# Kernel optimization log

Measured on AMD Instinct MI355X. Metric: run time of the kernel, lower is better.

Reference implementation:

```python
import jax, jax.numpy as jnp
import numpy as np

B, N, D, K = 16, 1024, 512, 32
EPS = 1e-12  # F.normalize default eps


def setup_inputs() -> dict:
    key = jax.random.key(0)
    k1, k2, k3 = jax.random.split(key, 3)
    x = jax.random.normal(k1, (B, N, D), dtype=jnp.float32)
    mask = (jax.random.uniform(k2, (B, N)) < 0.9).astype(jnp.float32)
    centroids = jax.random.uniform(k3, (D, K), dtype=jnp.float32)
    # _init_params: conv.weight = 2*alpha*centroids, conv.bias = -alpha*||centroids||_col
    W = 2.0 * centroids
    b = -jnp.linalg.norm(centroids, axis=0)
    return {"x": x, "mask": mask, "W": W, "b": b, "centroids": centroids}


def reference(x, mask, W, b, centroids):
    # descriptor-wise L2 normalization (normalize_input=True)
    xn = x / jnp.maximum(jnp.linalg.norm(x, axis=2, keepdims=True), EPS)
    # 1x1 conv (matmul) + bias, masked logits
    logits = (jnp.einsum('bnd,dk->bnk', xn, W) + b) * mask[:, :, None]
    soft_assign = jax.nn.softmax(logits, axis=2) * mask[:, :, None]  # (B,N,K)
    # entropy with -log2(0) -> 0 (matches log_p[isinf]=0 since sa*0 = 0 there)
    safe = jnp.where(soft_assign > 0, soft_assign, 1.0)
    assign_entropy = -(soft_assign * jnp.log2(safe)).sum() / mask.sum()
    # cluster-usage distribution
    assign_sum = soft_assign.sum(axis=1)  # (B,K)
    assign_dist = jax.nn.log_softmax(assign_sum, axis=1)
    # NetVLAD residual pooling, algebraically fused (avoids (B,N,D,K) tensor):
    # vlad[b,d,k] = sum_n xn*sa - centroids[d,k]*sum_n sa
    vlad = jnp.einsum('bnd,bnk->bdk', xn, soft_assign) - centroids[None] * assign_sum[:, None, :]
    vlad = vlad / jnp.maximum(jnp.linalg.norm(vlad, axis=1, keepdims=True), EPS)
    vlad = jnp.transpose(vlad, (0, 2, 1))  # (B,K,D)
    return (vlad, assign_dist, assign_entropy)
```

## Files before the change

kernel.cpp:

```cpp
#include <hip/hip_runtime.h>
#include <math.h>

#define B 16
#define N 1024
#define D 512
#define K 32
#define EPSF 1e-12f

#define WS_TT_F   0
#define WS_ASP_F  262144
#define WS_ENTP_F 294912
#define WS_MSKP_F 295936
#define WS_PART_F 296960

#define OFF_DIST 262144
#define OFF_ENT  262656

typedef __attribute__((ext_vector_type(8))) short s16x8;
typedef __attribute__((ext_vector_type(4))) short s16x4;
typedef __attribute__((ext_vector_type(4))) float f32x4;

__device__ __forceinline__ ushort f2b(float f) {
    unsigned u = __builtin_bit_cast(unsigned, f);
    u += 0x7fffu + ((u >> 16) & 1u);
    return (ushort)(u >> 16);
}

__global__ __launch_bounds__(256) void kA(const float* __restrict__ x,
    const float* __restrict__ mask, const float* __restrict__ Wf,
    const float* __restrict__ bias, float* __restrict__ ws)
{
    __shared__ ushort wtl[32 * 512];
    __shared__ ushort xs[4 * 16 * 128];
    __shared__ float4 accsh[2 * 128];
    __shared__ float ssqsh[2 * 16];
    __shared__ float invsh[2 * 16];
    const int bid = blockIdx.x;
    const int b = bid >> 5;
    const int s = bid & 31;
    const int tid = threadIdx.x;
    const int w = tid >> 6;
    const int rw = w & 1, dw = w >> 1;
    const int l = tid & 63;
    const int g = l >> 4, lo = l & 15;
    const int n0 = s * 32 + rw * 16;
    const int p = bid * 2 + rw;

    {
        const float4* Wg = (const float4*)Wf;
        #pragma unroll
        for (int i = 0; i < 16; ++i) {
            int f4 = tid + i * 256;
            float4 v = Wg[f4];
            int d = f4 >> 3, k4 = (f4 & 7) << 2;
            float vv[4] = {v.x, v.y, v.z, v.w};
            #pragma unroll
            for (int j = 0; j < 4; ++j) {
                int k = k4 + j;
                wtl[(k * 512 + d) ^ ((k & 7) << 3)] = f2b(vv[j]);
            }
        }
    }

    ushort* xw = xs + w * 2048;
    float ssq[8] = {0.f, 0.f, 0.f, 0.f, 0.f, 0.f, 0.f, 0.f};
    f32x4 acc[2] = {{0.f, 0.f, 0.f, 0.f}, {0.f, 0.f, 0.f, 0.f}};
    const float4* xg = (const float4*)(x + (size_t)(b * N + n0) * D);
    __syncthreads();

    #pragma unroll
    for (int cc = 0; cc < 2; ++cc) {
        const int c = dw * 2 + cc;
        float4 fv[8];
        #pragma unroll
        for (int j = 0; j < 8; ++j) {
            int idx = l + 64 * j;
            fv[j] = xg[(idx >> 5) * 128 + c * 32 + (idx & 31)];
        }
        #pragma unroll
        for (int j = 0; j < 8; ++j)
            ssq[j] += fv[j].x * fv[j].x + fv[j].y * fv[j].y
                    + fv[j].z * fv[j].z + fv[j].w * fv[j].w;
        #pragma unroll
        for (int j = 0; j < 8; ++j) {
            int idx = l + 64 * j;
            int r = idx >> 5, c4 = idx & 31;
            unsigned bo = (unsigned)(c4 * 8) ^ (unsigned)((r & 7) << 4);
            s16x4 sv = { (short)f2b(fv[j].x), (short)f2b(fv[j].y),
                         (short)f2b(fv[j].z), (short)f2b(fv[j].w) };
            *(s16x4*)&xw[r * 128 + (bo >> 1)] = sv;
        }
        __syncthreads();
        #pragma unroll
        for (int ks = 0; ks < 4; ++ks) {
            unsigned bo = (unsigned)(ks * 64 + g * 16) ^ (unsigned)((lo & 7) << 4);
            s16x8 bfrag = *(const s16x8*)&xw[lo * 128 + (bo >> 1)];
            int dglob = c * 128 + ks * 32 + g * 8;
            s16x8 a0 = *(const s16x8*)&wtl[(lo * 512 + dglob) ^ ((lo & 7) << 3)];
            s16x8 a1 = *(const s16x8*)&wtl[((16 + lo) * 512 + dglob) ^ ((lo & 7) << 3)];
            acc[0] = __builtin_amdgcn_mfma_f32_16x16x32_bf16(a0, bfrag, acc[0], 0, 0, 0);
            acc[1] = __builtin_amdgcn_mfma_f32_16x16x32_bf16(a1, bfrag, acc[1], 0, 0, 0);
        }
        __syncthreads();
    }

    #pragma unroll
    for (int j = 0; j < 8; ++j) {
        #pragma unroll
        for (int m = 16; m; m >>= 1) ssq[j] += __shfl_xor(ssq[j], m);
    }
    if (dw == 1) {
        if ((l & 31) == 0) {
            #pragma unroll
            for (int j = 0; j < 8; ++j)
                ssqsh[rw * 16 + (l >> 5) + 2 * j] = ssq[j];
        }
        accsh[rw * 128 + l * 2 + 0] = *(float4*)&acc[0];
        accsh[rw * 128 + l * 2 + 1] = *(float4*)&acc[1];
    }
    __syncthreads();
    if (dw == 0) {
        float4 o0 = accsh[rw * 128 + l * 2 + 0];
        float4 o1 = accsh[rw * 128 + l * 2 + 1];
        acc[0][0] += o0.x; acc[0][1] += o0.y; acc[0][2] += o0.z; acc[0][3] += o0.w;
        acc[1][0] += o1.x; acc[1][1] += o1.y; acc[1][2] += o1.z; acc[1][3] += o1.w;
        if ((l & 31) == 0) {
            #pragma unroll
            for (int j = 0; j < 8; ++j) {
                int r = (l >> 5) + 2 * j;
                invsh[rw * 16 + r] = 1.f / fmaxf(sqrtf(ssq[j] + ssqsh[rw * 16 + r]), EPSF);
            }
        }
    }
    __syncthreads();
    float sa[2][4];
    if (dw == 0) {
        const float inv = invsh[rw * 16 + lo];
        const float mv = mask[b * N + n0 + lo];
        float lg[2][4];
        #pragma unroll
        for (int kt = 0; kt < 2; ++kt)
            #pragma unroll
            for (int r = 0; r < 4; ++r)
                lg[kt][r] = (acc[kt][r] * inv + bias[kt * 16 + g * 4 + r]) * mv;
        float mx = lg[0][0];
        #pragma unroll
        for (int kt = 0; kt < 2; ++kt)
            #pragma unroll
            for (int r = 0; r < 4; ++r) mx = fmaxf(mx, lg[kt][r]);
        mx = fmaxf(mx, __shfl_xor(mx, 16));
        mx = fmaxf(mx, __shfl_xor(mx, 32));
        float e[2][4], sum = 0.f;
        #pragma unroll
        for (int kt = 0; kt < 2; ++kt)
            #pragma unroll
            for (int r = 0; r < 4; ++r) { e[kt][r] = __expf(lg[kt][r] - mx); sum += e[kt][r]; }
        sum += __shfl_xor(sum, 16);
        sum += __shfl_xor(sum, 32);
        const float rs = mv / sum;
        float ent = 0.f;
        #pragma unroll
        for (int kt = 0; kt < 2; ++kt)
            #pragma unroll
            for (int r = 0; r < 4; ++r) {
                sa[kt][r] = e[kt][r] * rs;
                ent += sa[kt][r] > 0.f ? -sa[kt][r] * __log2f(sa[kt][r]) : 0.f;
            }
        #pragma unroll
        for (int m = 32; m; m >>= 1) ent += __shfl_xor(ent, m);
        if (l == 0) ws[WS_ENTP_F + p] = ent;
        float mp = mv;
        #pragma unroll
        for (int m = 8; m; m >>= 1) mp += __shfl_xor(mp, m);
        if (l == 0) ws[WS_MSKP_F + p] = mp;
        #pragma unroll
        for (int kt = 0; kt < 2; ++kt)
            #pragma unroll
            for (int r = 0; r < 4; ++r) {
                float av = sa[kt][r];
                #pragma unroll
                for (int m = 8; m; m >>= 1) av += __shfl_xor(av, m);
                if (lo == 0) ws[WS_ASP_F + p * 32 + kt * 16 + g * 4 + r] = av;
            }
        #pragma unroll
        for (int kt = 0; kt < 2; ++kt)
            #pragma unroll
            for (int r = 0; r < 4; ++r)
                xw[(kt * 16 + g * 4 + r) * 16 + lo] = f2b(sa[kt][r] * inv);
    }
    __syncthreads();
    if (dw == 0) {
        ushort* tTg = (ushort*)ws;
        s16x8 tv = *(const s16x8*)&xw[l * 8];
        *(s16x8*)(tTg + (size_t)(b * 32 + (l >> 1)) * 1024 + n0 + (l & 1) * 8) = tv;
    }
}

__global__ __launch_bounds__(256) void kB(const float* __restrict__ x,
    const float* __restrict__ ws, float* __restrict__ parts)
{
    const int bid = blockIdx.x;
    const int b = bid >> 5;
    const int s = (bid >> 2) & 7;
    const int dh = bid & 3;
    const int w = threadIdx.x >> 6;
    const int l = threadIdx.x & 63;
    const int g = l >> 4, lo = l & 15;
    const int d0 = dh * 128 + w * 32;
    const ushort* tT = (const ushort*)ws;

    f32x4 acc[2][2] = {{{0.f,0.f,0.f,0.f},{0.f,0.f,0.f,0.f}},
                       {{0.f,0.f,0.f,0.f},{0.f,0.f,0.f,0.f}}};
    for (int ks = 0; ks < 4; ++ks) {
        int nb = s * 128 + ks * 32 + g * 8;
        s16x8 av[2];
        av[0] = *(const s16x8*)(tT + (size_t)(b * 32 + lo) * 1024 + nb);
        av[1] = *(const s16x8*)(tT + (size_t)(b * 32 + 16 + lo) * 1024 + nb);
        s16x8 bv[2];
        #pragma unroll
        for (int dt = 0; dt < 2; ++dt)
            #pragma unroll
            for (int j = 0; j < 8; ++j)
                bv[dt][j] = (short)f2b(x[(size_t)(b * N + nb + j) * 512 + d0 + dt * 16 + lo]);
        #pragma unroll
        for (int kt = 0; kt < 2; ++kt)
            #pragma unroll
            for (int dt = 0; dt < 2; ++dt)
                acc[kt][dt] = __builtin_amdgcn_mfma_f32_16x16x32_bf16(av[kt], bv[dt], acc[kt][dt], 0, 0, 0);
    }
    #pragma unroll
    for (int kt = 0; kt < 2; ++kt)
        #pragma unroll
        for (int dt = 0; dt < 2; ++dt)
            #pragma unroll
            for (int r = 0; r < 4; ++r) {
                int k = kt * 16 + g * 4 + r;
                int d = d0 + dt * 16 + lo;
                parts[((size_t)(s * 16 + b) * 32 + k) * 512 + d] = acc[kt][dt][r];
            }
}

__global__ __launch_bounds__(256) void kC(const float* __restrict__ cent,
    const float* __restrict__ ws, float* __restrict__ out)
{
    __shared__ float pm[256];
    __shared__ float asL[32];
    __shared__ float red[4];
    __shared__ float scs;
    const int bid = blockIdx.x;
    const int b = bid >> 5, k = bid & 31;
    const int t = threadIdx.x;
    {
        int kk = t & 31, i = t >> 5;
        float a = 0.f;
        #pragma unroll
        for (int ii = 0; ii < 8; ++ii)
            a += ws[WS_ASP_F + (size_t)(b * 64 + ii * 8 + i) * 32 + kk];
        pm[t] = a;
    }
    __syncthreads();
    if (t < 32) {
        float a = 0.f;
        #pragma unroll
        for (int i = 0; i < 8; ++i) a += pm[i * 32 + t];
        asL[t] = a;
    }
    __syncthreads();
    if (k == 0 && t < 32) {
        float a = asL[t];
        float mx = a;
        #pragma unroll
        for (int m = 16; m; m >>= 1) mx = fmaxf(mx, __shfl_xor(mx, m));
        float e = __expf(a - mx), ssum = e;
        #pragma unroll
        for (int m = 16; m; m >>= 1) ssum += __shfl_xor(ssum, m);
        out[OFF_DIST + b * 32 + t] = a - mx - logf(ssum);
    }
    if (bid == 0 && (t >> 6) == 1) {
        int l = t & 63;
        float es = 0.f, ms = 0.f;
        for (int i = l; i < 1024; i += 64) {
            es += ws[WS_ENTP_F + i];
            ms += ws[WS_MSKP_F + i];
        }
        #pragma unroll
        for (int m = 32; m; m >>= 1) { es += __shfl_xor(es, m); ms += __shfl_xor(ms, m); }
        if (l == 0) out[OFF_ENT] = es / ms;
    }
    const float as = asL[k];
    float v0 = 0.f, v1 = 0.f;
    #pragma unroll
    for (int s = 0; s < 8; ++s) {
        const float* pp = ws + WS_PART_F + ((size_t)(s * 16 + b) * 32 + k) * 512;
        v0 += pp[t];
        v1 += pp[t + 256];
    }
    v0 -= cent[t * 32 + k] * as;
    v1 -= cent[(t + 256) * 32 + k] * as;
    float ss = v0 * v0 + v1 * v1;
    #pragma unroll
    for (int m = 32; m; m >>= 1) ss += __shfl_xor(ss, m);
    if ((t & 63) == 0) red[t >> 6] = ss;
    __syncthreads();
    if (t == 0) scs = 1.f / fmaxf(sqrtf(red[0] + red[1] + red[2] + red[3]), EPSF);
    __syncthreads();
    out[(size_t)(b * 32 + k) * 512 + t] = v0 * scs;
    out[(size_t)(b * 32 + k) * 512 + t + 256] = v1 * scs;
}

extern "C" void kernel_launch(void* const* d_in, const int* in_sizes, int n_in,
                              void* d_out, int out_size, void* d_ws, size_t ws_size,
                              hipStream_t stream)
{
    const float* x    = (const float*)d_in[0];
    const float* mask = (const float*)d_in[1];
    const float* W    = (const float*)d_in[2];
    const float* bias = (const float*)d_in[3];
    const float* cent = (const float*)d_in[4];
    float* out = (float*)d_out;
    float* ws  = (float*)d_ws;

    kA<<<dim3(512), dim3(256), 0, stream>>>(x, mask, W, bias, ws);
    kB<<<dim3(512), dim3(256), 0, stream>>>(x, ws, ws + WS_PART_F);
    kC<<<dim3(512), dim3(256), 0, stream>>>(cent, ws, out);
}
```

Measured before the change: 33.99 us.

## Fuse VLAD aggregation into assignment kernel and precompute transposed weights

Moves the xn·soft_assign aggregation into the first kernel using a transposed bf16 copy of the x tile kept in LDS, eliminating the separate kernel that re-read x from global memory. A small prep kernel converts W to bf16 [K][D] and transposes centroids once, so kA no longer rebuilds the weight tile in LDS per block. Partials are now stored as bf16 with 32 splits and reduced in a narrower final kernel with vectorized loads. This trades higher LDS usage, more partial traffic and bf16 rounding of partial sums for removing a full pass over x.

```diff
diff --git a/kernel.cpp b/kernel.cpp
--- a/kernel.cpp
+++ b/kernel.cpp
@@ -7,11 +7,12 @@
 #define K 32
 #define EPSF 1e-12f
 
-#define WS_TT_F   0
-#define WS_ASP_F  262144
-#define WS_ENTP_F 294912
-#define WS_MSKP_F 295936
-#define WS_PART_F 296960
+#define WS_WT_F   0
+#define WS_CT_F   8192
+#define WS_ASP_F  24576
+#define WS_ENTP_F 57344
+#define WS_MSKP_F 58368
+#define WS_PART_F 59392
 
 #define OFF_DIST 262144
 #define OFF_ENT  262656
@@ -25,16 +26,49 @@
     u += 0x7fffu + ((u >> 16) & 1u);
     return (ushort)(u >> 16);
 }
-
-__global__ __launch_bounds__(256) void kA(const float* __restrict__ x,
-    const float* __restrict__ mask, const float* __restrict__ Wf,
-    const float* __restrict__ bias, float* __restrict__ ws)
+__device__ __forceinline__ float b2f(ushort u) {
+    return __builtin_bit_cast(float, (unsigned)u << 16);
+}
+
+__global__ __launch_bounds__(256) void k0_prep(const float* __restrict__ Wf,
+    const float* __restrict__ cent, float* __restrict__ ws)
 {
-    __shared__ ushort wtl[32 * 512];
-    __shared__ ushort xs[4 * 16 * 128];
+    const int t = threadIdx.x;
+    const int kk = t >> 3, dseg = (t & 7) * 64;
+    if (blockIdx.x == 0) {
+        ushort* wt = (ushort*)(ws + WS_WT_F);
+        #pragma unroll
+        for (int d8 = 0; d8 < 8; ++d8) {
+            s16x8 v;
+            #pragma unroll
+            for (int e = 0; e < 8; ++e)
+                v[e] = f2b(Wf[(dseg + d8 * 8 + e) * 32 + kk]);
+            *(s16x8*)(wt + kk * 512 + dseg + d8 * 8) = v;
+        }
+    } else {
+        float* ct = ws + WS_CT_F;
+        #pragma unroll
+        for (int d4 = 0; d4 < 16; ++d4) {
+            float4 v;
+            v.x = cent[(dseg + d4 * 4 + 0) * 32 + kk];
+            v.y = cent[(dseg + d4 * 4 + 1) * 32 + kk];
+            v.z = cent[(dseg + d4 * 4 + 2) * 32 + kk];
+            v.w = cent[(dseg + d4 * 4 + 3) * 32 + kk];
+            *(float4*)(ct + kk * 512 + dseg + d4 * 4) = v;
+        }
+    }
+}
+
+__global__ __launch_bounds__(256, 2) void kA(const float* __restrict__ x,
+    const float* __restrict__ mask, const float* __restrict__ bias,
+    float* __restrict__ ws, ushort* __restrict__ parts)
+{
+    __shared__ ushort xs[4 * 2048];
+    __shared__ ushort xsT[512 * 36];
+    __shared__ ushort tls[32 * 32];
     __shared__ float4 accsh[2 * 128];
-    __shared__ float ssqsh[2 * 16];
-    __shared__ float invsh[2 * 16];
+    __shared__ float ssqsh[32], invsh[32];
+
     const int bid = blockIdx.x;
     const int b = bid >> 5;
     const int s = bid & 31;
@@ -45,28 +79,12 @@
     const int g = l >> 4, lo = l & 15;
     const int n0 = s * 32 + rw * 16;
     const int p = bid * 2 + rw;
-
-    {
-        const float4* Wg = (const float4*)Wf;
-        #pragma unroll
-        for (int i = 0; i < 16; ++i) {
-            int f4 = tid + i * 256;
-            float4 v = Wg[f4];
-            int d = f4 >> 3, k4 = (f4 & 7) << 2;
-            float vv[4] = {v.x, v.y, v.z, v.w};
-            #pragma unroll
-            for (int j = 0; j < 4; ++j) {
-                int k = k4 + j;
-                wtl[(k * 512 + d) ^ ((k & 7) << 3)] = f2b(vv[j]);
-            }
-        }
-    }
+    const ushort* wt = (const ushort*)(ws + WS_WT_F);
 
     ushort* xw = xs + w * 2048;
     float ssq[8] = {0.f, 0.f, 0.f, 0.f, 0.f, 0.f, 0.f, 0.f};
     f32x4 acc[2] = {{0.f, 0.f, 0.f, 0.f}, {0.f, 0.f, 0.f, 0.f}};
     const float4* xg = (const float4*)(x + (size_t)(b * N + n0) * D);
-    __syncthreads();
 
     #pragma unroll
     for (int cc = 0; cc < 2; ++cc) {
@@ -89,19 +107,23 @@
             s16x4 sv = { (short)f2b(fv[j].x), (short)f2b(fv[j].y),
                          (short)f2b(fv[j].z), (short)f2b(fv[j].w) };
             *(s16x4*)&xw[r * 128 + (bo >> 1)] = sv;
-        }
-        __syncthreads();
+            int nn = rw * 16 + r;
+            int dbase = c * 128 + c4 * 4;
+            xsT[(dbase + 0) * 36 + nn] = (ushort)sv[0];
+            xsT[(dbase + 1) * 36 + nn] = (ushort)sv[1];
+            xsT[(dbase + 2) * 36 + nn] = (ushort)sv[2];
+            xsT[(dbase + 3) * 36 + nn] = (ushort)sv[3];
+        }
         #pragma unroll
         for (int ks = 0; ks < 4; ++ks) {
             unsigned bo = (unsigned)(ks * 64 + g * 16) ^ (unsigned)((lo & 7) << 4);
             s16x8 bfrag = *(const s16x8*)&xw[lo * 128 + (bo >> 1)];
             int dglob = c * 128 + ks * 32 + g * 8;
-            s16x8 a0 = *(const s16x8*)&wtl[(lo * 512 + dglob) ^ ((lo & 7) << 3)];
-            s16x8 a1 = *(const s16x8*)&wtl[((16 + lo) * 512 + dglob) ^ ((lo & 7) << 3)];
+            s16x8 a0 = *(const s16x8*)(wt + (size_t)lo * 512 + dglob);
+            s16x8 a1 = *(const s16x8*)(wt + (size_t)(16 + lo) * 512 + dglob);
             acc[0] = __builtin_amdgcn_mfma_f32_16x16x32_bf16(a0, bfrag, acc[0], 0, 0, 0);
             acc[1] = __builtin_amdgcn_mfma_f32_16x16x32_bf16(a1, bfrag, acc[1], 0, 0, 0);
         }
-        __syncthreads();
     }
 
     #pragma unroll
@@ -133,7 +155,6 @@
         }
     }
     __syncthreads();
-    float sa[2][4];
     if (dw == 0) {
         const float inv = invsh[rw * 16 + lo];
         const float mv = mask[b * N + n0 + lo];
@@ -158,7 +179,7 @@
         sum += __shfl_xor(sum, 16);
         sum += __shfl_xor(sum, 32);
         const float rs = mv / sum;
-        float ent = 0.f;
+        float sa[2][4], ent = 0.f;
         #pragma unroll
         for (int kt = 0; kt < 2; ++kt)
             #pragma unroll
@@ -186,67 +207,55 @@
         for (int kt = 0; kt < 2; ++kt)
             #pragma unroll
             for (int r = 0; r < 4; ++r)
-                xw[(kt * 16 + g * 4 + r) * 16 + lo] = f2b(sa[kt][r] * inv);
-    }
-    __syncthreads();
-    if (dw == 0) {
-        ushort* tTg = (ushort*)ws;
-        s16x8 tv = *(const s16x8*)&xw[l * 8];
-        *(s16x8*)(tTg + (size_t)(b * 32 + (l >> 1)) * 1024 + n0 + (l & 1) * 8) = tv;
-    }
-}
-
-__global__ __launch_bounds__(256) void kB(const float* __restrict__ x,
-    const float* __restrict__ ws, float* __restrict__ parts)
+                tls[(kt * 16 + g * 4 + r) * 32 + rw * 16 + lo] = f2b(sa[kt][r] * inv);
+    }
+    __syncthreads();
+
+    f32x4 acc2[2][8];
+    #pragma unroll
+    for (int kt = 0; kt < 2; ++kt)
+        #pragma unroll
+        for (int dt = 0; dt < 8; ++dt)
+            acc2[kt][dt] = (f32x4){0.f, 0.f, 0.f, 0.f};
+    {
+        s16x8 av0 = *(const s16x8*)&tls[lo * 32 + g * 8];
+        s16x8 av1 = *(const s16x8*)&tls[(16 + lo) * 32 + g * 8];
+        #pragma unroll
+        for (int dt = 0; dt < 8; ++dt) {
+            int d = w * 128 + dt * 16 + lo;
+            s16x4 b0 = *(const s16x4*)&xsT[d * 36 + g * 8];
+            s16x4 b1 = *(const s16x4*)&xsT[d * 36 + g * 8 + 4];
+            s16x8 bv;
+            bv[0] = b0[0]; bv[1] = b0[1]; bv[2] = b0[2]; bv[3] = b0[3];
+            bv[4] = b1[0]; bv[5] = b1[1]; bv[6] = b1[2]; bv[7] = b1[3];
+            acc2[0][dt] = __builtin_amdgcn_mfma_f32_16x16x32_bf16(av0, bv, acc2[0][dt], 0, 0, 0);
+            acc2[1][dt] = __builtin_amdgcn_mfma_f32_16x16x32_bf16(av1, bv, acc2[1][dt], 0, 0, 0);
+        }
+    }
+    __syncthreads();
+    ushort* stg = xsT;
+    #pragma unroll
+    for (int kt = 0; kt < 2; ++kt)
+        #pragma unroll
+        for (int dt = 0; dt < 8; ++dt)
+            #pragma unroll
+            for (int r = 0; r < 4; ++r)
+                stg[(kt * 16 + g * 4 + r) * 520 + w * 128 + dt * 16 + lo] = f2b(acc2[kt][dt][r]);
+    __syncthreads();
+    #pragma unroll
+    for (int j = 0; j < 8; ++j) {
+        int k = w * 8 + j;
+        s16x8 v = *(const s16x8*)&stg[k * 520 + l * 8];
+        *(s16x8*)(parts + ((size_t)(s * 16 + b) * 32 + k) * 512 + l * 8) = v;
+    }
+}
+
+__global__ __launch_bounds__(128) void kC(const float* __restrict__ ws,
+    const ushort* __restrict__ parts, float* __restrict__ out)
 {
-    const int bid = blockIdx.x;
-    const int b = bid >> 5;
-    const int s = (bid >> 2) & 7;
-    const int dh = bid & 3;
-    const int w = threadIdx.x >> 6;
-    const int l = threadIdx.x & 63;
-    const int g = l >> 4, lo = l & 15;
-    const int d0 = dh * 128 + w * 32;
-    const ushort* tT = (const ushort*)ws;
-
-    f32x4 acc[2][2] = {{{0.f,0.f,0.f,0.f},{0.f,0.f,0.f,0.f}},
-                       {{0.f,0.f,0.f,0.f},{0.f,0.f,0.f,0.f}}};
-    for (int ks = 0; ks < 4; ++ks) {
-        int nb = s * 128 + ks * 32 + g * 8;
-        s16x8 av[2];
-        av[0] = *(const s16x8*)(tT + (size_t)(b * 32 + lo) * 1024 + nb);
-        av[1] = *(const s16x8*)(tT + (size_t)(b * 32 + 16 + lo) * 1024 + nb);
-        s16x8 bv[2];
-        #pragma unroll
-        for (int dt = 0; dt < 2; ++dt)
-            #pragma unroll
-            for (int j = 0; j < 8; ++j)
-                bv[dt][j] = (short)f2b(x[(size_t)(b * N + nb + j) * 512 + d0 + dt * 16 + lo]);
-        #pragma unroll
-        for (int kt = 0; kt < 2; ++kt)
-            #pragma unroll
-            for (int dt = 0; dt < 2; ++dt)
-                acc[kt][dt] = __builtin_amdgcn_mfma_f32_16x16x32_bf16(av[kt], bv[dt], acc[kt][dt], 0, 0, 0);
-    }
-    #pragma unroll
-    for (int kt = 0; kt < 2; ++kt)
-        #pragma unroll
-        for (int dt = 0; dt < 2; ++dt)
-            #pragma unroll
-            for (int r = 0; r < 4; ++r) {
-                int k = kt * 16 + g * 4 + r;
-                int d = d0 + dt * 16 + lo;
-                parts[((size_t)(s * 16 + b) * 32 + k) * 512 + d] = acc[kt][dt][r];
-            }
-}
-
-__global__ __launch_bounds__(256) void kC(const float* __restrict__ cent,
-    const float* __restrict__ ws, float* __restrict__ out)
-{
-    __shared__ float pm[256];
+    __shared__ float pm[128];
     __shared__ float asL[32];
-    __shared__ float red[4];
-    __shared__ float scs;
+    __shared__ float red[2];
     const int bid = blockIdx.x;
     const int b = bid >> 5, k = bid & 31;
     const int t = threadIdx.x;
@@ -254,15 +263,15 @@
         int kk = t & 31, i = t >> 5;
         float a = 0.f;
         #pragma unroll
-        for (int ii = 0; ii < 8; ++ii)
-            a += ws[WS_ASP_F + (size_t)(b * 64 + ii * 8 + i) * 32 + kk];
+        for (int ii = 0; ii < 16; ++ii)
+            a += ws[WS_ASP_F + (size_t)(b * 64 + ii * 4 + i) * 32 + kk];
         pm[t] = a;
     }
     __syncthreads();
     if (t < 32) {
         float a = 0.f;
         #pragma unroll
-        for (int i = 0; i < 8; ++i) a += pm[i * 32 + t];
+        for (int i = 0; i < 4; ++i) a += pm[i * 32 + t];
         asL[t] = a;
     }
     __syncthreads();
@@ -287,25 +296,29 @@
         for (int m = 32; m; m >>= 1) { es += __shfl_xor(es, m); ms += __shfl_xor(ms, m); }
         if (l == 0) out[OFF_ENT] = es / ms;
     }
+    const int d0 = t * 4;
+    float a0 = 0.f, a1 = 0.f, a2 = 0.f, a3 = 0.f;
+    for (int s = 0; s < 32; ++s) {
+        s16x4 v = *(const s16x4*)(parts + ((size_t)(s * 16 + b) * 32 + k) * 512 + d0);
+        a0 += b2f((ushort)v[0]);
+        a1 += b2f((ushort)v[1]);
+        a2 += b2f((ushort)v[2]);
+        a3 += b2f((ushort)v[3]);
+    }
     const float as = asL[k];
-    float v0 = 0.f, v1 = 0.f;
-    #pragma unroll
-    for (int s = 0; s < 8; ++s) {
-        const float* pp = ws + WS_PART_F + ((size_t)(s * 16 + b) * 32 + k) * 512;
-        v0 += pp[t];
-        v1 += pp[t + 256];
-    }
-    v0 -= cent[t * 32 + k] * as;
-    v1 -= cent[(t + 256) * 32 + k] * as;
-    float ss = v0 * v0 + v1 * v1;
-    #pragma unroll
-    for (int m = 32; m; m >>= 1) ss += __shfl_xor(ss, m);
-    if ((t & 63) == 0) red[t >> 6] = ss;
-    __syncthreads();
-    if (t == 0) scs = 1.f / fmaxf(sqrtf(red[0] + red[1] + red[2] + red[3]), EPSF);
-    __syncthreads();
-    out[(size_t)(b * 32 + k) * 512 + t] = v0 * scs;
-    out[(size_t)(b * 32 + k) * 512 + t + 256] = v1 * scs;
+    float4 ct = *(const float4*)(ws + WS_CT_F + k * 512 + d0);
+    float v0 = a0 - ct.x * as;
+    float v1 = a1 - ct.y * as;
+    float v2 = a2 - ct.z * as;
+    float v3 = a3 - ct.w * as;
+    float sq = v0 * v0 + v1 * v1 + v2 * v2 + v3 * v3;
+    #pragma unroll
+    for (int m = 32; m; m >>= 1) sq += __shfl_xor(sq, m);
+    if ((t & 63) == 0) red[t >> 6] = sq;
+    __syncthreads();
+    float sc = 1.f / fmaxf(sqrtf(red[0] + red[1]), EPSF);
+    float4 o = make_float4(v0 * sc, v1 * sc, v2 * sc, v3 * sc);
+    *(float4*)(out + (size_t)(b * 32 + k) * 512 + d0) = o;
 }
 
 extern "C" void kernel_launch(void* const* d_in, const int* in_sizes, int n_in,
@@ -319,8 +332,9 @@
     const float* cent = (const float*)d_in[4];
     float* out = (float*)d_out;
     float* ws  = (float*)d_ws;
-
-    kA<<<dim3(512), dim3(256), 0, stream>>>(x, mask, W, bias, ws);
-    kB<<<dim3(512), dim3(256), 0, stream>>>(x, ws, ws + WS_PART_F);
-    kC<<<dim3(512), dim3(256), 0, stream>>>(cent, ws, out);
-}
+    ushort* parts = (ushort*)(ws + WS_PART_F);
+
+    k0_prep<<<dim3(2), dim3(256), 0, stream>>>(W, cent, ws);
+    kA<<<dim3(512), dim3(256), 0, stream>>>(x, mask, bias, ws, parts);
+    kC<<<dim3(512), dim3(128), 0, stream>>>(ws, parts, out);
+}
```

New measurement: 36.04 us. 6.0% more time.
